# Optimization experiments

Measured on AMD Instinct MI355X. Metric: run time of the kernel, lower is better.

The kernel has to match this reference:

```python
import jax, jax.numpy as jnp
import numpy as np

N_NODES = 50000
N_EDGES = 800000
NODE_DIM = 32
EDGE_DIM = 16
HIDDEN = 64


def setup_inputs() -> dict:
    key = jax.random.key(0)
    ks = jax.random.split(key, 7)
    h = jax.random.normal(ks[0], (N_NODES, HIDDEN), dtype=jnp.float32)
    nf = jax.random.normal(ks[1], (N_NODES, NODE_DIM), dtype=jnp.float32)
    ef = jax.random.normal(ks[2], (N_EDGES, EDGE_DIM), dtype=jnp.float32)
    src = jax.random.randint(ks[3], (N_EDGES,), 0, N_NODES, dtype=jnp.int32)
    dst = jax.random.randint(ks[4], (N_EDGES,), 0, N_NODES, dtype=jnp.int32)
    # torch Linear weights: [out_features, in_features]
    in1 = HIDDEN + 2 * NODE_DIM + EDGE_DIM  # 144
    W1 = jax.random.normal(ks[5], (HIDDEN, in1), dtype=jnp.float32) * (1.0 / np.sqrt(in1))
    W2 = jax.random.normal(ks[6], (HIDDEN, HIDDEN), dtype=jnp.float32) * (1.0 / np.sqrt(HIDDEN))
    return {"h": h, "nf": nf, "ef": ef, "src": src, "dst": dst, "W1": W1, "W2": W2}


def reference(h, nf, ef, src, dst, W1, W2):
    n = nf.shape[0]
    # per-edge message: concat(dst.x, edge.x, src.h)  -> [E, node+edge+hidden]
    m_e = jnp.concatenate([nf[dst], ef, h[src]], axis=-1)
    # mailbox sum per destination node
    m = jax.ops.segment_sum(m_e, dst, num_segments=n)  # [N, node+edge+hidden]
    z = jnp.concatenate([nf, m], axis=-1)              # [N, hidden+2*node+edge]
    new_h = jax.nn.relu(z @ W1.T) @ W2.T               # [N, hidden]
    # DGL update_all only updates nodes that received at least one message
    deg = jax.ops.segment_sum(jnp.ones_like(dst, dtype=jnp.float32), dst, num_segments=n)
    return jnp.where(deg[:, None] > 0, new_h, h)
```

## Files before the change

### kernel.cpp

```cpp
#include <hip/hip_runtime.h>

#define NDIM 32
#define EDIM 16
#define NHID 64
#define NIN1 144
#define SCHUNK 1024
#define SPT 4

__device__ __forceinline__ unsigned pk2(float a, float b) {
  unsigned ua = __float_as_uint(a);
  unsigned ub = __float_as_uint(b);
  ua = (ua + 0x7FFFu + ((ua >> 16) & 1u)) >> 16;
  ub = (ub + 0x7FFFu + ((ub >> 16) & 1u)) >> 16;
  return ua | (ub << 16);
}
__device__ __forceinline__ float lo16(unsigned u) { return __uint_as_float(u << 16); }
__device__ __forceinline__ float hi16(unsigned u) { return __uint_as_float(u & 0xFFFF0000u); }

#define ACC8(A, V)                                   \
  do {                                               \
    A[0] += lo16((V).x); A[1] += hi16((V).x);        \
    A[2] += lo16((V).y); A[3] += hi16((V).y);        \
    A[4] += lo16((V).z); A[5] += hi16((V).z);        \
    A[6] += lo16((V).w); A[7] += hi16((V).w);        \
  } while (0)

__global__ __launch_bounds__(256) void sse_conv(
    const float* __restrict__ h, uint4* __restrict__ h16,
    const float* __restrict__ W1, float* __restrict__ W1T,
    const float* __restrict__ W2, float* __restrict__ W2T, int N) {
  int t = blockIdx.x * 256 + threadIdx.x;
  int T = gridDim.x * 256;
  if (t < NHID * NIN1) {
    int r = t / NIN1, k = t - r * NIN1;
    W1T[k * NHID + r] = W1[t];
  } else if (t < NHID * NIN1 + NHID * NHID) {
    int i = t - NHID * NIN1;
    int r = i >> 6, k = i & 63;
    W2T[k * NHID + r] = W2[i];
  }
  const float4* hf4 = (const float4*)h;
  int NH = N * 8;
  for (int i = t; i < NH; i += T) {
    float4 x = hf4[2 * i], y = hf4[2 * i + 1];
    uint4 o;
    o.x = pk2(x.x, x.y); o.y = pk2(x.z, x.w);
    o.z = pk2(y.x, y.y); o.w = pk2(y.z, y.w);
    h16[i] = o;
  }
}

__global__ __launch_bounds__(256) void sse_hist(
    const int* __restrict__ dst, int* __restrict__ counts,
    int* __restrict__ rank, int E) {
  int ebase = blockIdx.x * 1024 + threadIdx.x;
  int r[4];
#pragma unroll
  for (int i = 0; i < 4; ++i) {
    int e = ebase + i * 256;
    if (e < E) r[i] = atomicAdd(&counts[dst[e]], 1);
  }
#pragma unroll
  for (int i = 0; i < 4; ++i) {
    int e = ebase + i * 256;
    if (e < E) rank[e] = r[i];
  }
}

__global__ __launch_bounds__(256) void sse_scan_part(
    const int* __restrict__ counts, int* __restrict__ bsum, int N) {
  __shared__ int ws[4];
  int t = threadIdx.x;
  int base = blockIdx.x * SCHUNK + t * SPT;
  int s = 0;
#pragma unroll
  for (int i = 0; i < SPT; ++i) {
    int idx = base + i;
    if (idx < N) s += counts[idx];
  }
  int v = s;
#pragma unroll
  for (int off = 1; off < 64; off <<= 1) v += __shfl_xor(v, off, 64);
  if ((t & 63) == 0) ws[t >> 6] = v;
  __syncthreads();
  if (t == 0) bsum[blockIdx.x] = ws[0] + ws[1] + ws[2] + ws[3];
}

__global__ __launch_bounds__(256) void sse_scan_final(
    const int* __restrict__ counts, const int* __restrict__ bsum,
    int* __restrict__ starts, int N, int nb) {
  __shared__ int ws[4];
  int t = threadIdx.x;
  int lane = t & 63, w = t >> 6;
  int boff = 0;
  for (int j = 0; j < (int)blockIdx.x; ++j) boff += bsum[j];
  int base = blockIdx.x * SCHUNK + t * SPT;
  int c[SPT];
  int s = 0;
#pragma unroll
  for (int i = 0; i < SPT; ++i) {
    int idx = base + i;
    c[i] = (idx < N) ? counts[idx] : 0;
    s += c[i];
  }
  int incl = s;
#pragma unroll
  for (int off = 1; off < 64; off <<= 1) {
    int u = __shfl_up(incl, off, 64);
    if (lane >= off) incl += u;
  }
  if (lane == 63) ws[w] = incl;
  __syncthreads();
  int woff = 0;
#pragma unroll
  for (int j = 0; j < 4; ++j)
    if (j < w) woff += ws[j];
  int run = boff + woff + (incl - s);
#pragma unroll
  for (int i = 0; i < SPT; ++i) {
    int idx = base + i;
    if (idx < N) {
      starts[idx] = run;
      run += c[i];
    }
  }
  if ((int)blockIdx.x == nb - 1 && t == 0)
    starts[N] = boff + ws[0] + ws[1] + ws[2] + ws[3];
}

__global__ __launch_bounds__(256) void sse_build(
    const int* __restrict__ src, const int* __restrict__ dst,
    const int* __restrict__ rank, const int* __restrict__ starts,
    int2* __restrict__ sedge, int E) {
  int ebase = blockIdx.x * 1024 + threadIdx.x;
#pragma unroll
  for (int i = 0; i < 4; ++i) {
    int e = ebase + i * 256;
    if (e < E) {
      int d = dst[e];
      int pos = starts[d] + rank[e];
      sedge[pos] = make_int2(src[e], e);
    }
  }
}

__global__ __launch_bounds__(256) void sse_gather(
    const uint4* __restrict__ h16, const float* __restrict__ ef,
    const int2* __restrict__ sedge, const int* __restrict__ starts,
    uint4* __restrict__ efsum16, uint4* __restrict__ hsum16, int N) {
  int w = threadIdx.x >> 6;
  int lane = threadIdx.x & 63;
  int node = blockIdx.x * 4 + w;
  if (node >= N) return;
  int st = starts[node], en = starts[node + 1];

  const float4* ef4 = (const float4*)ef;
  int q8 = lane >> 3, m = lane & 7;
  int eq = lane >> 2, em = lane & 3;

  float acc[8];
#pragma unroll
  for (int i = 0; i < 8; ++i) acc[i] = 0.f;
  float4 ea = make_float4(0.f, 0.f, 0.f, 0.f);

  for (int base = st; base < en; base += 64) {
    int C = en - base; C = C > 64 ? 64 : C;
    int2 seg = (lane < C) ? sedge[base + lane] : make_int2(0, 0);
    int myS = seg.x, myE = seg.y;
    int nr = (C + 31) >> 5;
    for (int r = 0; r < nr; ++r) {
      int b = r * 32;
      int i0 = b + q8, i1 = b + 8 + q8, i2 = b + 16 + q8, i3 = b + 24 + q8;
      int s0 = __shfl(myS, i0, 64);
      int s1 = __shfl(myS, i1, 64);
      int s2 = __shfl(myS, i2, 64);
      int s3 = __shfl(myS, i3, 64);
      int e0 = b + eq, e1 = b + 16 + eq;
      int id0 = __shfl(myE, e0, 64);
      int id1 = __shfl(myE, e1, 64);
      uint4 v0 = h16[(size_t)s0 * 8 + m];
      uint4 v1 = h16[(size_t)s1 * 8 + m];
      uint4 v2 = h16[(size_t)s2 * 8 + m];
      uint4 v3 = h16[(size_t)s3 * 8 + m];
      float4 x0 = ef4[(size_t)id0 * 4 + em];
      float4 x1 = ef4[(size_t)id1 * 4 + em];
      if (i0 < C) ACC8(acc, v0);
      if (i1 < C) ACC8(acc, v1);
      if (i2 < C) ACC8(acc, v2);
      if (i3 < C) ACC8(acc, v3);
      if (e0 < C) { ea.x += x0.x; ea.y += x0.y; ea.z += x0.z; ea.w += x0.w; }
      if (e1 < C) { ea.x += x1.x; ea.y += x1.y; ea.z += x1.z; ea.w += x1.w; }
    }
  }

#pragma unroll
  for (int off = 8; off < 64; off <<= 1)
#pragma unroll
    for (int i = 0; i < 8; ++i) acc[i] += __shfl_xor(acc[i], off, 64);
  if (lane < 8) {
    uint4 o;
    o.x = pk2(acc[0], acc[1]); o.y = pk2(acc[2], acc[3]);
    o.z = pk2(acc[4], acc[5]); o.w = pk2(acc[6], acc[7]);
    hsum16[(size_t)node * 8 + lane] = o;
  }
#pragma unroll
  for (int off = 4; off < 64; off <<= 1) {
    ea.x += __shfl_xor(ea.x, off, 64);
    ea.y += __shfl_xor(ea.y, off, 64);
    ea.z += __shfl_xor(ea.z, off, 64);
    ea.w += __shfl_xor(ea.w, off, 64);
  }
  float bx = __shfl_xor(ea.x, 1, 64);
  float by = __shfl_xor(ea.y, 1, 64);
  float bz = __shfl_xor(ea.z, 1, 64);
  float bw = __shfl_xor(ea.w, 1, 64);
  if (lane < 4 && (lane & 1) == 0) {
    uint4 o;
    o.x = pk2(ea.x, ea.y); o.y = pk2(ea.z, ea.w);
    o.z = pk2(bx, by);     o.w = pk2(bz, bw);
    efsum16[(size_t)node * 2 + (lane >> 1)] = o;
  }
}

__global__ __launch_bounds__(256) void sse_node(
    const float* __restrict__ h, const float* __restrict__ nf,
    const uint4* __restrict__ efsum16, const uint4* __restrict__ hsum16,
    const int* __restrict__ starts, const float* __restrict__ W1T,
    const float* __restrict__ W2T, float* __restrict__ out, int N) {
  __shared__ float4 zs[36 * 64];
  __shared__ float4 as[16 * 64];

  int tid = threadIdx.x;
  int lane = tid & 63;
  int w = __builtin_amdgcn_readfirstlane(tid) >> 6;

  int node = blockIdx.x * 64 + lane;
  int nodeC = node < N ? node : N - 1;

  if (w == 0) {
    int st = starts[nodeC], en = starts[nodeC + 1];
    float dg = (float)(en - st);
    const float4* nfr = (const float4*)(nf + (size_t)nodeC * NDIM);
#pragma unroll
    for (int k4 = 0; k4 < 8; ++k4) {
      float4 v = nfr[k4];
      zs[k4 * 64 + lane] = v;
      zs[(8 + k4) * 64 + lane] =
          make_float4(dg * v.x, dg * v.y, dg * v.z, dg * v.w);
    }
  } else if (w == 1) {
    uint4 a = efsum16[(size_t)nodeC * 2 + 0];
    uint4 b = efsum16[(size_t)nodeC * 2 + 1];
    zs[16 * 64 + lane] = make_float4(lo16(a.x), hi16(a.x), lo16(a.y), hi16(a.y));
    zs[17 * 64 + lane] = make_float4(lo16(a.z), hi16(a.z), lo16(a.w), hi16(a.w));
    zs[18 * 64 + lane] = make_float4(lo16(b.x), hi16(b.x), lo16(b.y), hi16(b.y));
    zs[19 * 64 + lane] = make_float4(lo16(b.z), hi16(b.z), lo16(b.w), hi16(b.w));
  } else if (w == 2) {
#pragma unroll
    for (int c = 0; c < 4; ++c) {
      uint4 u = hsum16[(size_t)nodeC * 8 + c];
      zs[(20 + 2 * c) * 64 + lane] =
          make_float4(lo16(u.x), hi16(u.x), lo16(u.y), hi16(u.y));
      zs[(21 + 2 * c) * 64 + lane] =
          make_float4(lo16(u.z), hi16(u.z), lo16(u.w), hi16(u.w));
    }
  } else {
#pragma unroll
    for (int c = 4; c < 8; ++c) {
      uint4 u = hsum16[(size_t)nodeC * 8 + c];
      zs[(20 + 2 * c) * 64 + lane] =
          make_float4(lo16(u.x), hi16(u.x), lo16(u.y), hi16(u.y));
      zs[(21 + 2 * c) * 64 + lane] =
          make_float4(lo16(u.z), hi16(u.z), lo16(u.w), hi16(u.w));
    }
  }
  __syncthreads();

  const float4* w1b = (const float4*)W1T + w * 4;
  float a[16];
#pragma unroll
  for (int j = 0; j < 16; ++j) a[j] = 0.f;

#pragma unroll 2
  for (int k4 = 0; k4 < 36; ++k4) {
    float4 zv = zs[k4 * 64 + lane];
#pragma unroll
    for (int kk = 0; kk < 4; ++kk) {
      int k = k4 * 4 + kk;
      float4 w0 = w1b[k * 16 + 0];
      float4 w1 = w1b[k * 16 + 1];
      float4 w2 = w1b[k * 16 + 2];
      float4 w3 = w1b[k * 16 + 3];
      float zk = kk == 0 ? zv.x : kk == 1 ? zv.y : kk == 2 ? zv.z : zv.w;
      a[0]  = fmaf(w0.x, zk, a[0]);
      a[1]  = fmaf(w0.y, zk, a[1]);
      a[2]  = fmaf(w0.z, zk, a[2]);
      a[3]  = fmaf(w0.w, zk, a[3]);
      a[4]  = fmaf(w1.x, zk, a[4]);
      a[5]  = fmaf(w1.y, zk, a[5]);
      a[6]  = fmaf(w1.z, zk, a[6]);
      a[7]  = fmaf(w1.w, zk, a[7]);
      a[8]  = fmaf(w2.x, zk, a[8]);
      a[9]  = fmaf(w2.y, zk, a[9]);
      a[10] = fmaf(w2.z, zk, a[10]);
      a[11] = fmaf(w2.w, zk, a[11]);
      a[12] = fmaf(w3.x, zk, a[12]);
      a[13] = fmaf(w3.y, zk, a[13]);
      a[14] = fmaf(w3.z, zk, a[14]);
      a[15] = fmaf(w3.w, zk, a[15]);
    }
  }

#pragma unroll
  for (int j4 = 0; j4 < 4; ++j4)
    as[(w * 4 + j4) * 64 + lane] =
        make_float4(fmaxf(a[j4 * 4 + 0], 0.f), fmaxf(a[j4 * 4 + 1], 0.f),
                    fmaxf(a[j4 * 4 + 2], 0.f), fmaxf(a[j4 * 4 + 3], 0.f));
  __syncthreads();

  const float4* w2b = (const float4*)W2T + w * 4;
  float o[16];
#pragma unroll
  for (int j = 0; j < 16; ++j) o[j] = 0.f;

#pragma unroll 2
  for (int kq = 0; kq < 16; ++kq) {
    float4 av = as[kq * 64 + lane];
#pragma unroll
    for (int kk = 0; kk < 4; ++kk) {
      int k = kq * 4 + kk;
      float4 w0 = w2b[k * 16 + 0];
      float4 w1 = w2b[k * 16 + 1];
      float4 w2 = w2b[k * 16 + 2];
      float4 w3 = w2b[k * 16 + 3];
      float ak = kk == 0 ? av.x : kk == 1 ? av.y : kk == 2 ? av.z : av.w;
      o[0]  = fmaf(w0.x, ak, o[0]);
      o[1]  = fmaf(w0.y, ak, o[1]);
      o[2]  = fmaf(w0.z, ak, o[2]);
      o[3]  = fmaf(w0.w, ak, o[3]);
      o[4]  = fmaf(w1.x, ak, o[4]);
      o[5]  = fmaf(w1.y, ak, o[5]);
      o[6]  = fmaf(w1.z, ak, o[6]);
      o[7]  = fmaf(w1.w, ak, o[7]);
      o[8]  = fmaf(w2.x, ak, o[8]);
      o[9]  = fmaf(w2.y, ak, o[9]);
      o[10] = fmaf(w2.z, ak, o[10]);
      o[11] = fmaf(w2.w, ak, o[11]);
      o[12] = fmaf(w3.x, ak, o[12]);
      o[13] = fmaf(w3.y, ak, o[13]);
      o[14] = fmaf(w3.z, ak, o[14]);
      o[15] = fmaf(w3.w, ak, o[15]);
    }
  }

  if (node < N) {
    int st = starts[node], en = starts[node + 1];
    float4* o4 = (float4*)(out + (size_t)node * NHID + w * 16);
    if (en - st == 0) {
      const float4* hr = (const float4*)(h + (size_t)node * NHID + w * 16);
#pragma unroll
      for (int j4 = 0; j4 < 4; ++j4) o4[j4] = hr[j4];
    } else {
#pragma unroll
      for (int j4 = 0; j4 < 4; ++j4)
        o4[j4] = make_float4(o[j4 * 4 + 0], o[j4 * 4 + 1], o[j4 * 4 + 2],
                             o[j4 * 4 + 3]);
    }
  }
}

extern "C" void kernel_launch(void* const* d_in, const int* in_sizes, int n_in,
                              void* d_out, int out_size, void* d_ws, size_t ws_size,
                              hipStream_t stream) {
  const float* h  = (const float*)d_in[0];
  const float* nf = (const float*)d_in[1];
  const float* ef = (const float*)d_in[2];
  const int*   src = (const int*)d_in[3];
  const int*   dst = (const int*)d_in[4];
  const float* W1 = (const float*)d_in[5];
  const float* W2 = (const float*)d_in[6];
  float* out = (float*)d_out;

  int N = in_sizes[0] / NHID;
  int E = in_sizes[3];

  char* p = (char*)d_ws;
  int2* sedge = (int2*)p;                 p += (size_t)E * 8;
  int* counts = (int*)p;                  p += (size_t)N * 4;
  int* starts = (int*)p;                  p += (size_t)(N + 1) * 4;
  int* bsum = (int*)p;                    p += 64 * 4;
  float* W1T = (float*)p;                 p += (size_t)NIN1 * NHID * 4;
  float* W2T = (float*)p;                 p += (size_t)NHID * NHID * 4;
  p = (char*)(((size_t)p + 15) & ~(size_t)15);
  uint4* h16 = (uint4*)p;                 p += (size_t)N * 128;
  uint4* efsum16 = (uint4*)p;             p += (size_t)N * 32;
  uint4* hsum16 = (uint4*)p;              p += (size_t)N * 128;
  int* rank = (int*)hsum16;

  hipMemsetAsync(counts, 0, (size_t)N * sizeof(int), stream);

  int eblocks4 = (E + 1023) / 1024;
  int nb = (N + SCHUNK - 1) / SCHUNK;

  sse_conv<<<1024, 256, 0, stream>>>(h, h16, W1, W1T, W2, W2T, N);
  sse_hist<<<eblocks4, 256, 0, stream>>>(dst, counts, rank, E);
  sse_scan_part<<<nb, 256, 0, stream>>>(counts, bsum, N);
  sse_scan_final<<<nb, 256, 0, stream>>>(counts, bsum, starts, N, nb);
  sse_build<<<eblocks4, 256, 0, stream>>>(src, dst, rank, starts, sedge, E);

  int gblocks = (N + 3) / 4;
  sse_gather<<<gblocks, 256, 0, stream>>>(h16, ef, sedge, starts,
                                          efsum16, hsum16, N);

  int nblocks = (N + 63) / 64;
  sse_node<<<nblocks, 256, 0, stream>>>(h, nf, efsum16, hsum16, starts, W1T,
                                        W2T, out, N);
}
```

Before: 232.3 us.

## Fuse conversion into histogram kernel and issue all gather loads up front

```diff
diff --git a/kernel.cpp b/kernel.cpp
--- a/kernel.cpp
+++ b/kernel.cpp
@@ -6,6 +6,7 @@
 #define NIN1 144
 #define SCHUNK 1024
 #define SPT 4
+#define SBLK 128
 
 __device__ __forceinline__ unsigned pk2(float a, float b) {
   unsigned ua = __float_as_uint(a);
@@ -25,45 +26,47 @@
     A[6] += lo16((V).w); A[7] += hi16((V).w);        \
   } while (0)
 
-__global__ __launch_bounds__(256) void sse_conv(
-    const float* __restrict__ h, uint4* __restrict__ h16,
-    const float* __restrict__ W1, float* __restrict__ W1T,
-    const float* __restrict__ W2, float* __restrict__ W2T, int N) {
-  int t = blockIdx.x * 256 + threadIdx.x;
-  int T = gridDim.x * 256;
-  if (t < NHID * NIN1) {
-    int r = t / NIN1, k = t - r * NIN1;
-    W1T[k * NHID + r] = W1[t];
-  } else if (t < NHID * NIN1 + NHID * NHID) {
-    int i = t - NHID * NIN1;
-    int r = i >> 6, k = i & 63;
-    W2T[k * NHID + r] = W2[i];
-  }
-  const float4* hf4 = (const float4*)h;
-  int NH = N * 8;
-  for (int i = t; i < NH; i += T) {
-    float4 x = hf4[2 * i], y = hf4[2 * i + 1];
-    uint4 o;
-    o.x = pk2(x.x, x.y); o.y = pk2(x.z, x.w);
-    o.z = pk2(y.x, y.y); o.w = pk2(y.z, y.w);
-    h16[i] = o;
-  }
-}
-
 __global__ __launch_bounds__(256) void sse_hist(
     const int* __restrict__ dst, int* __restrict__ counts,
-    int* __restrict__ rank, int E) {
-  int ebase = blockIdx.x * 1024 + threadIdx.x;
-  int r[4];
-#pragma unroll
-  for (int i = 0; i < 4; ++i) {
-    int e = ebase + i * 256;
-    if (e < E) r[i] = atomicAdd(&counts[dst[e]], 1);
-  }
-#pragma unroll
-  for (int i = 0; i < 4; ++i) {
-    int e = ebase + i * 256;
-    if (e < E) rank[e] = r[i];
+    int* __restrict__ rank,
+    const float* __restrict__ W1, float* __restrict__ W1T,
+    const float* __restrict__ W2, float* __restrict__ W2T,
+    const float* __restrict__ h, uint4* __restrict__ h16,
+    int E, int N, int eblocks) {
+  int b = blockIdx.x;
+  if (b < eblocks) {
+    int ebase = b * 1024 + threadIdx.x;
+    int r[4];
+#pragma unroll
+    for (int i = 0; i < 4; ++i) {
+      int e = ebase + i * 256;
+      if (e < E) r[i] = atomicAdd(&counts[dst[e]], 1);
+    }
+#pragma unroll
+    for (int i = 0; i < 4; ++i) {
+      int e = ebase + i * 256;
+      if (e < E) rank[e] = r[i];
+    }
+  } else {
+    int t = (b - eblocks) * 256 + threadIdx.x;
+    int T = SBLK * 256;
+    if (t < NHID * NIN1) {
+      int rr = t / NIN1, k = t - rr * NIN1;
+      W1T[k * NHID + rr] = W1[t];
+    } else if (t < NHID * NIN1 + NHID * NHID) {
+      int i = t - NHID * NIN1;
+      int rr = i >> 6, k = i & 63;
+      W2T[k * NHID + rr] = W2[i];
+    }
+    const float4* hf4 = (const float4*)h;
+    int NH = N * 8;
+    for (int i = t; i < NH; i += T) {
+      float4 x = hf4[2 * i], y = hf4[2 * i + 1];
+      uint4 o;
+      o.x = pk2(x.x, x.y); o.y = pk2(x.z, x.w);
+      o.z = pk2(y.x, y.y); o.w = pk2(y.z, y.w);
+      h16[i] = o;
+    }
   }
 }
 
@@ -167,30 +170,29 @@
     int C = en - base; C = C > 64 ? 64 : C;
     int2 seg = (lane < C) ? sedge[base + lane] : make_int2(0, 0);
     int myS = seg.x, myE = seg.y;
-    int nr = (C + 31) >> 5;
-    for (int r = 0; r < nr; ++r) {
-      int b = r * 32;
-      int i0 = b + q8, i1 = b + 8 + q8, i2 = b + 16 + q8, i3 = b + 24 + q8;
-      int s0 = __shfl(myS, i0, 64);
-      int s1 = __shfl(myS, i1, 64);
-      int s2 = __shfl(myS, i2, 64);
-      int s3 = __shfl(myS, i3, 64);
-      int e0 = b + eq, e1 = b + 16 + eq;
-      int id0 = __shfl(myE, e0, 64);
-      int id1 = __shfl(myE, e1, 64);
-      uint4 v0 = h16[(size_t)s0 * 8 + m];
-      uint4 v1 = h16[(size_t)s1 * 8 + m];
-      uint4 v2 = h16[(size_t)s2 * 8 + m];
-      uint4 v3 = h16[(size_t)s3 * 8 + m];
-      float4 x0 = ef4[(size_t)id0 * 4 + em];
-      float4 x1 = ef4[(size_t)id1 * 4 + em];
-      if (i0 < C) ACC8(acc, v0);
-      if (i1 < C) ACC8(acc, v1);
-      if (i2 < C) ACC8(acc, v2);
-      if (i3 < C) ACC8(acc, v3);
-      if (e0 < C) { ea.x += x0.x; ea.y += x0.y; ea.z += x0.z; ea.w += x0.w; }
-      if (e1 < C) { ea.x += x1.x; ea.y += x1.y; ea.z += x1.z; ea.w += x1.w; }
-    }
+
+    int hs[8];
+#pragma unroll
+    for (int g = 0; g < 8; ++g) hs[g] = __shfl(myS, g * 8 + q8, 64);
+    int eid[4];
+#pragma unroll
+    for (int j = 0; j < 4; ++j) eid[j] = __shfl(myE, j * 16 + eq, 64);
+
+    uint4 hv[8];
+#pragma unroll
+    for (int g = 0; g < 8; ++g) hv[g] = h16[(size_t)hs[g] * 8 + m];
+    float4 ev[4];
+#pragma unroll
+    for (int j = 0; j < 4; ++j) ev[j] = ef4[(size_t)eid[j] * 4 + em];
+
+#pragma unroll
+    for (int g = 0; g < 8; ++g)
+      if (g * 8 + q8 < C) ACC8(acc, hv[g]);
+#pragma unroll
+    for (int j = 0; j < 4; ++j)
+      if (j * 16 + eq < C) {
+        ea.x += ev[j].x; ea.y += ev[j].y; ea.z += ev[j].z; ea.w += ev[j].w;
+      }
   }
 
 #pragma unroll
@@ -402,8 +404,9 @@
   int eblocks4 = (E + 1023) / 1024;
   int nb = (N + SCHUNK - 1) / SCHUNK;
 
-  sse_conv<<<1024, 256, 0, stream>>>(h, h16, W1, W1T, W2, W2T, N);
-  sse_hist<<<eblocks4, 256, 0, stream>>>(dst, counts, rank, E);
+  sse_hist<<<eblocks4 + SBLK, 256, 0, stream>>>(dst, counts, rank, W1, W1T,
+                                                W2, W2T, h, h16, E, N,
+                                                eblocks4);
   sse_scan_part<<<nb, 256, 0, stream>>>(counts, bsum, N);
   sse_scan_final<<<nb, 256, 0, stream>>>(counts, bsum, starts, N, nb);
   sse_build<<<eblocks4, 256, 0, stream>>>(src, dst, rank, starts, sedge, E);
```

Result: slower. 239.2 us (+3.0%).

## Fuse bf16 conversion into histogram kernel and use single-block scan

Applied to the files above, without the earlier changes.

```diff
diff --git a/kernel.cpp b/kernel.cpp
--- a/kernel.cpp
+++ b/kernel.cpp
@@ -4,8 +4,7 @@
 #define EDIM 16
 #define NHID 64
 #define NIN1 144
-#define SCHUNK 1024
-#define SPT 4
+#define SBLK 128
 
 __device__ __forceinline__ unsigned pk2(float a, float b) {
   unsigned ua = __float_as_uint(a);
@@ -25,107 +24,83 @@
     A[6] += lo16((V).w); A[7] += hi16((V).w);        \
   } while (0)
 
-__global__ __launch_bounds__(256) void sse_conv(
-    const float* __restrict__ h, uint4* __restrict__ h16,
-    const float* __restrict__ W1, float* __restrict__ W1T,
-    const float* __restrict__ W2, float* __restrict__ W2T, int N) {
-  int t = blockIdx.x * 256 + threadIdx.x;
-  int T = gridDim.x * 256;
-  if (t < NHID * NIN1) {
-    int r = t / NIN1, k = t - r * NIN1;
-    W1T[k * NHID + r] = W1[t];
-  } else if (t < NHID * NIN1 + NHID * NHID) {
-    int i = t - NHID * NIN1;
-    int r = i >> 6, k = i & 63;
-    W2T[k * NHID + r] = W2[i];
-  }
-  const float4* hf4 = (const float4*)h;
-  int NH = N * 8;
-  for (int i = t; i < NH; i += T) {
-    float4 x = hf4[2 * i], y = hf4[2 * i + 1];
-    uint4 o;
-    o.x = pk2(x.x, x.y); o.y = pk2(x.z, x.w);
-    o.z = pk2(y.x, y.y); o.w = pk2(y.z, y.w);
-    h16[i] = o;
-  }
-}
-
 __global__ __launch_bounds__(256) void sse_hist(
     const int* __restrict__ dst, int* __restrict__ counts,
-    int* __restrict__ rank, int E) {
-  int ebase = blockIdx.x * 1024 + threadIdx.x;
-  int r[4];
-#pragma unroll
-  for (int i = 0; i < 4; ++i) {
-    int e = ebase + i * 256;
-    if (e < E) r[i] = atomicAdd(&counts[dst[e]], 1);
-  }
-#pragma unroll
-  for (int i = 0; i < 4; ++i) {
-    int e = ebase + i * 256;
-    if (e < E) rank[e] = r[i];
-  }
-}
-
-__global__ __launch_bounds__(256) void sse_scan_part(
-    const int* __restrict__ counts, int* __restrict__ bsum, int N) {
-  __shared__ int ws[4];
+    int* __restrict__ rank,
+    const float* __restrict__ W1, float* __restrict__ W1T,
+    const float* __restrict__ W2, float* __restrict__ W2T,
+    const float* __restrict__ h, uint4* __restrict__ h16,
+    int E, int N, int eblocks) {
+  int b = blockIdx.x;
+  if (b < eblocks) {
+    int ebase = b * 1024 + threadIdx.x;
+    int r[4];
+#pragma unroll
+    for (int i = 0; i < 4; ++i) {
+      int e = ebase + i * 256;
+      if (e < E) r[i] = atomicAdd(&counts[dst[e]], 1);
+    }
+#pragma unroll
+    for (int i = 0; i < 4; ++i) {
+      int e = ebase + i * 256;
+      if (e < E) rank[e] = r[i];
+    }
+  } else {
+    int t = (b - eblocks) * 256 + threadIdx.x;
+    int T = SBLK * 256;
+    if (t < NHID * NIN1) {
+      int rr = t / NIN1, k = t - rr * NIN1;
+      W1T[k * NHID + rr] = W1[t];
+    } else if (t < NHID * NIN1 + NHID * NHID) {
+      int i = t - NHID * NIN1;
+      int rr = i >> 6, k = i & 63;
+      W2T[k * NHID + rr] = W2[i];
+    }
+    const float4* hf4 = (const float4*)h;
+    int NH = N * 8;
+    for (int i = t; i < NH; i += T) {
+      float4 x = hf4[2 * i], y = hf4[2 * i + 1];
+      uint4 o;
+      o.x = pk2(x.x, x.y); o.y = pk2(x.z, x.w);
+      o.z = pk2(y.x, y.y); o.w = pk2(y.z, y.w);
+      h16[i] = o;
+    }
+  }
+}
+
+__global__ __launch_bounds__(1024) void sse_scan(
+    const int* __restrict__ counts, int* __restrict__ starts, int N) {
+  __shared__ int wsum[16];
+  __shared__ int carry;
   int t = threadIdx.x;
-  int base = blockIdx.x * SCHUNK + t * SPT;
-  int s = 0;
-#pragma unroll
-  for (int i = 0; i < SPT; ++i) {
-    int idx = base + i;
-    if (idx < N) s += counts[idx];
-  }
-  int v = s;
-#pragma unroll
-  for (int off = 1; off < 64; off <<= 1) v += __shfl_xor(v, off, 64);
-  if ((t & 63) == 0) ws[t >> 6] = v;
+  int lane = t & 63, wv = t >> 6;
+  if (t == 0) carry = 0;
   __syncthreads();
-  if (t == 0) bsum[blockIdx.x] = ws[0] + ws[1] + ws[2] + ws[3];
-}
-
-__global__ __launch_bounds__(256) void sse_scan_final(
-    const int* __restrict__ counts, const int* __restrict__ bsum,
-    int* __restrict__ starts, int N, int nb) {
-  __shared__ int ws[4];
-  int t = threadIdx.x;
-  int lane = t & 63, w = t >> 6;
-  int boff = 0;
-  for (int j = 0; j < (int)blockIdx.x; ++j) boff += bsum[j];
-  int base = blockIdx.x * SCHUNK + t * SPT;
-  int c[SPT];
-  int s = 0;
-#pragma unroll
-  for (int i = 0; i < SPT; ++i) {
-    int idx = base + i;
-    c[i] = (idx < N) ? counts[idx] : 0;
-    s += c[i];
-  }
-  int incl = s;
-#pragma unroll
-  for (int off = 1; off < 64; off <<= 1) {
-    int u = __shfl_up(incl, off, 64);
-    if (lane >= off) incl += u;
-  }
-  if (lane == 63) ws[w] = incl;
-  __syncthreads();
-  int woff = 0;
-#pragma unroll
-  for (int j = 0; j < 4; ++j)
-    if (j < w) woff += ws[j];
-  int run = boff + woff + (incl - s);
-#pragma unroll
-  for (int i = 0; i < SPT; ++i) {
-    int idx = base + i;
-    if (idx < N) {
-      starts[idx] = run;
-      run += c[i];
-    }
-  }
-  if ((int)blockIdx.x == nb - 1 && t == 0)
-    starts[N] = boff + ws[0] + ws[1] + ws[2] + ws[3];
+  for (int base = 0; base < N; base += 1024) {
+    int idx = base + t;
+    int c = (idx < N) ? counts[idx] : 0;
+    int incl = c;
+#pragma unroll
+    for (int o = 1; o < 64; o <<= 1) {
+      int u = __shfl_up(incl, o, 64);
+      if (lane >= o) incl += u;
+    }
+    if (lane == 63) wsum[wv] = incl;
+    __syncthreads();
+    int woff = 0, total = 0;
+#pragma unroll
+    for (int j = 0; j < 16; ++j) {
+      int v = wsum[j];
+      if (j < wv) woff += v;
+      total += v;
+    }
+    int cbase = carry;
+    if (idx < N) starts[idx] = cbase + woff + (incl - c);
+    __syncthreads();
+    if (t == 0) carry = cbase + total;
+    __syncthreads();
+  }
+  if (t == 0) starts[N] = carry;
 }
 
 __global__ __launch_bounds__(256) void sse_build(
@@ -388,7 +363,6 @@
   int2* sedge = (int2*)p;                 p += (size_t)E * 8;
   int* counts = (int*)p;                  p += (size_t)N * 4;
   int* starts = (int*)p;                  p += (size_t)(N + 1) * 4;
-  int* bsum = (int*)p;                    p += 64 * 4;
   float* W1T = (float*)p;                 p += (size_t)NIN1 * NHID * 4;
   float* W2T = (float*)p;                 p += (size_t)NHID * NHID * 4;
   p = (char*)(((size_t)p + 15) & ~(size_t)15);
@@ -400,12 +374,11 @@
   hipMemsetAsync(counts, 0, (size_t)N * sizeof(int), stream);
 
   int eblocks4 = (E + 1023) / 1024;
-  int nb = (N + SCHUNK - 1) / SCHUNK;
-
-  sse_conv<<<1024, 256, 0, stream>>>(h, h16, W1, W1T, W2, W2T, N);
-  sse_hist<<<eblocks4, 256, 0, stream>>>(dst, counts, rank, E);
-  sse_scan_part<<<nb, 256, 0, stream>>>(counts, bsum, N);
-  sse_scan_final<<<nb, 256, 0, stream>>>(counts, bsum, starts, N, nb);
+
+  sse_hist<<<eblocks4 + SBLK, 256, 0, stream>>>(dst, counts, rank, W1, W1T,
+                                                W2, W2T, h, h16, E, N,
+                                                eblocks4);
+  sse_scan<<<1, 1024, 0, stream>>>(counts, starts, N);
   sse_build<<<eblocks4, 256, 0, stream>>>(src, dst, rank, starts, sedge, E);
 
   int gblocks = (N + 3) / 4;
```

Result: slower. 269.3 us (+15.9%).
